# Kernel tuning notes

Measured on AMD Instinct MI355X. Metric: run time of the kernel, lower is better.

The kernel has to match this reference:

```python
import jax, jax.numpy as jnp
import numpy as np

N_EMBD = 1024
N_HEAD = 16
BLOCK_SIZE = 2048
NEG_INF = -1e10


def _rope_cache(head_dim, max_positions):
    # theta_i = 10000^{-2i/dim}, freqs[t, i] = t * theta_i
    theta = 1.0 / (10000.0 ** (jnp.arange(0, head_dim, 2, dtype=jnp.float32) / head_dim))
    freqs = jnp.arange(max_positions, dtype=jnp.float32)[:, None] * theta[None, :]
    return jnp.cos(freqs), jnp.sin(freqs)  # each (max_positions, head_dim//2)


def _apply_rope(x, cos, sin):
    # x: (B, nh, T, hs) interpreted as interleaved complex pairs
    B, nh, T, hs = x.shape
    xr = x.reshape(B, nh, T, hs // 2, 2)
    x0, x1 = xr[..., 0], xr[..., 1]
    c = cos[:T][None, None, :, :]
    s = sin[:T][None, None, :, :]
    o0 = x0 * c - x1 * s
    o1 = x0 * s + x1 * c
    return jnp.stack([o0, o1], axis=-1).reshape(B, nh, T, hs)


def setup_inputs() -> dict:
    key = jax.random.key(0)
    ks = jax.random.split(key, 9)
    B, T, C = 2, 2048, N_EMBD
    sc = 1.0 / np.sqrt(C)
    return {
        "x": jax.random.normal(ks[0], (B, T, C), jnp.float32),
        "Wq": jax.random.normal(ks[1], (C, C), jnp.float32) * sc,
        "bq": jax.random.normal(ks[2], (C,), jnp.float32) * 0.02,
        "Wk": jax.random.normal(ks[3], (C, C), jnp.float32) * sc,
        "bk": jax.random.normal(ks[4], (C,), jnp.float32) * 0.02,
        "Wv": jax.random.normal(ks[5], (C, C), jnp.float32) * sc,
        "bv": jax.random.normal(ks[6], (C,), jnp.float32) * 0.02,
        "Wp": jax.random.normal(ks[7], (C, C), jnp.float32) * sc,
        "bp": jax.random.normal(ks[8], (C,), jnp.float32) * 0.02,
    }


def reference(x, Wq, bq, Wk, bk, Wv, bv, Wp, bp):
    B, T, C = x.shape
    nh, hs = N_HEAD, C // N_HEAD

    def heads(W, b):
        return (x @ W.T + b).reshape(B, T, nh, hs).transpose(0, 2, 1, 3)

    q = heads(Wq, bq)
    k = heads(Wk, bk)
    v = heads(Wv, bv)

    cos, sin = _rope_cache(hs, BLOCK_SIZE)
    q = _apply_rope(q, cos, sin)
    k = _apply_rope(k, cos, sin)

    att = jnp.einsum("bhqd,bhkd->bhqk", q, k) * (1.0 / np.sqrt(hs))
    causal = jnp.tril(jnp.ones((T, T), dtype=bool))
    att = jnp.where(causal[None, None], att, NEG_INF)
    att = jax.nn.softmax(att, axis=-1)
    y = jnp.einsum("bhqk,bhkd->bhqd", att, v)
    y = y.transpose(0, 2, 1, 3).reshape(B, T, C)
    return y @ Wp.T + bp
```

## Files before the change

kernel.cpp:

```cpp
#include <hip/hip_runtime.h>

typedef __bf16 bf16;
typedef short  s16;
typedef s16   s16x8 __attribute__((ext_vector_type(8)));
typedef bf16  bf16x4 __attribute__((ext_vector_type(4)));
typedef float f32x4 __attribute__((ext_vector_type(4)));

#define B_SZ 2
#define T_SEQ 2048
#define C_DIM 1024
#define NH 16
#define HS 64
#define M_TOT (B_SZ * T_SEQ)

#define NEG_BIG (-30000.0f)
#define LOG2_10000 13.287712379549449f
#define Q_PRESCALE 0.18033688011112042f


__device__ __forceinline__ float san(float x) {
    unsigned u = __float_as_uint(x);
    return ((u & 0x7F800000u) == 0x7F800000u) ? 0.f : x;
}

__device__ __forceinline__ void load16_lds(const bf16* g, void* lds_base) {
    __builtin_amdgcn_global_load_lds(
        (const __attribute__((address_space(1))) void*)g,
        (__attribute__((address_space(3))) void*)lds_base, 16, 0, 0);
}

#define CVT_GRID 8448

__global__ __launch_bounds__(256) void cvt_bf16_kernel(
    const float* __restrict__ x,  const float* __restrict__ wq,
    const float* __restrict__ wk, const float* __restrict__ wv,
    const float* __restrict__ wp,
    bf16* __restrict__ xb, bf16* __restrict__ wqb, bf16* __restrict__ wkb,
    bf16* __restrict__ wvb, bf16* __restrict__ wpb,
    float* __restrict__ cs, float* __restrict__ sn)
{
    const int b = blockIdx.x;
    if (b >= 8192) {
        const int idx = (b - 8192) * 256 + threadIdx.x;
        const int t = idx >> 5, i = idx & 31;
        const float theta = __builtin_exp2f(-(float)(2 * i) * (LOG2_10000 / 64.f));
        const float a = (float)t * theta;
        cs[idx] = san(cosf(a));
        sn[idx] = san(sinf(a));
        return;
    }
    int z, base;
    if (b < 4096) { z = 0; base = b; }
    else          { z = 1 + ((b - 4096) >> 10); base = (b - 4096) & 1023; }

    const float* src = (z == 0) ? x : (z == 1) ? wq : (z == 2) ? wk : (z == 3) ? wv : wp;
    bf16* dst = (z == 0) ? xb : (z == 1) ? wqb : (z == 2) ? wkb : (z == 3) ? wvb : wpb;

    const int i = (base * 256 + threadIdx.x) * 4;
    const float4 v = *(const float4*)(src + i);
    bf16x4 o;
    o[0] = (bf16)v.x; o[1] = (bf16)v.y; o[2] = (bf16)v.z; o[3] = (bf16)v.w;
    *(bf16x4*)(dst + i) = o;
}

#define QSTAGE(bufi, kk)                                                       \
    load16_lds(gA + (kk),               (char*)(sA[bufi]) + w * 1024);         \
    load16_lds(gA + 128 * C_DIM + (kk), (char*)(sA[bufi]) + 8192 + w * 1024);  \
    load16_lds(gB + (kk),               (char*)(sB[bufi]) + w * 1024);         \
    load16_lds(gB + 128 * C_DIM + (kk), (char*)(sB[bufi]) + 8192 + w * 1024);

__global__ __launch_bounds__(512, 2) void qkv_gemm(
    const bf16* __restrict__ X, const bf16* __restrict__ W_all,
    const float* __restrict__ bq, const float* __restrict__ bk,
    const float* __restrict__ bv,
    const float* __restrict__ cs_tab, const float* __restrict__ sn_tab,
    bf16* __restrict__ q_ws, bf16* __restrict__ k_ws, bf16* __restrict__ vt_ws)
{
    __shared__ __attribute__((aligned(16))) bf16 sA[3][256 * 32];
    __shared__ __attribute__((aligned(16))) bf16 sB[3][256 * 32];

    const int m0 = blockIdx.x * 256;
    const int n0 = blockIdx.y * 256;
    const int mode = blockIdx.y >> 2;

    const int t = threadIdx.x;
    const int w = t >> 6;
    const int lane = t & 63;
    const int qd = lane >> 4;
    const int r  = lane & 15;
    const int qs = qd ^ ((r >> 1) & 3);
    const int wm = w >> 2, wn = w & 3;
    const int srow = t >> 2;
    const int scol = ((t & 3) ^ ((t >> 3) & 3)) * 8;
    const bf16* gA = X + (size_t)(m0 + srow) * C_DIM + scol;
    const bf16* gB = W_all + (size_t)(n0 + srow) * C_DIM + scol;

    f32x4 acc[8][4] = {};

    QSTAGE(0, 0)
    QSTAGE(1, 32)
    #pragma unroll
    for (int kt_ = 0; kt_ < 32; kt_++) {
        __builtin_amdgcn_sched_barrier(0);
        if (kt_ < 30) asm volatile("s_waitcnt vmcnt(4) lgkmcnt(0)" ::: "memory");
        else          asm volatile("s_waitcnt vmcnt(0) lgkmcnt(0)" ::: "memory");
        __builtin_amdgcn_sched_barrier(0);
        __builtin_amdgcn_s_barrier();
        __builtin_amdgcn_sched_barrier(0);
        if (kt_ + 2 < 32) { QSTAGE((kt_ + 2) % 3, (kt_ + 2) * 32) }
        {
            const bf16* pA = sA[kt_ % 3];
            const bf16* pB = sB[kt_ % 3];
            s16x8 af[8], bfr[4];
            #pragma unroll
            for (int mt = 0; mt < 8; mt++)
                af[mt] = *(const s16x8*)(pA + (wm * 128 + mt * 16 + r) * 32 + qs * 8);
            #pragma unroll
            for (int nt = 0; nt < 4; nt++)
                bfr[nt] = *(const s16x8*)(pB + (wn * 64 + nt * 16 + r) * 32 + qs * 8);
            #pragma unroll
            for (int mt = 0; mt < 8; mt++)
                #pragma unroll
                for (int nt = 0; nt < 4; nt++)
                    acc[mt][nt] = __builtin_amdgcn_mfma_f32_16x16x32_bf16(
                        af[mt], bfr[nt], acc[mt][nt], 0, 0, 0);
        }
    }

    const float* bias = (mode == 0) ? bq : (mode == 1) ? bk : bv;

    if (mode == 2) {
        #pragma unroll
        for (int mt = 0; mt < 8; mt++) {
            const int mrow0 = m0 + wm * 128 + mt * 16 + qd * 4;
            const int bb = mrow0 >> 11;
            const int t0 = mrow0 & 2047;
            #pragma unroll
            for (int nt = 0; nt < 4; nt++) {
                const int cm = (n0 & 1023) + wn * 64 + nt * 16 + r;
                const int h = cm >> 6, d = cm & 63;
                const float bv_ = bias[cm];
                bf16x4 pk;
                #pragma unroll
                for (int reg = 0; reg < 4; reg++)
                    pk[reg] = (bf16)san(acc[mt][nt][reg] + bv_);
                *(bf16x4*)(vt_ws + ((size_t)(bb * NH + h) * HS + d) * T_SEQ + t0) = pk;
            }
        }
    } else {
        bf16* out = (mode == 0) ? q_ws : k_ws;
        const float post = (mode == 0) ? Q_PRESCALE : 1.0f;
        #pragma unroll
        for (int mt = 0; mt < 8; mt++) {
            const int mrow0 = m0 + wm * 128 + mt * 16 + qd * 4;
            const int bb = mrow0 >> 11;
            const int t0 = mrow0 & 2047;
            #pragma unroll
            for (int nt = 0; nt < 4; nt++) {
                const int cm = (n0 & 1023) + wn * 64 + nt * 16 + r;
                const int h = cm >> 6, d = cm & 63;
                const int pi = d >> 1;
                const float bv_ = bias[cm];
                #pragma unroll
                for (int reg = 0; reg < 4; reg++) {
                    const int tt = t0 + reg;
                    float v = san(acc[mt][nt][reg] + bv_);
                    float partner = __shfl_xor(v, 1);
                    float c = cs_tab[tt * 32 + pi];
                    float s = sn_tab[tt * 32 + pi];
                    float rot = (d & 1) ? (v * c + partner * s)
                                        : (v * c - partner * s);
                    out[((size_t)(bb * NH + h) * T_SEQ + tt) * HS + d] =
                        (bf16)san(rot * post);
                }
            }
        }
    }
}

#define STAGE3(bufi, kk)                                                       \
    load16_lds(gA0 + (kk), (char*)(sA + (bufi) * 2048) + w * 1024);            \
    load16_lds(gB0 + (kk), (char*)(sB + (bufi) * 4096) + w * 1024);            \
    load16_lds(gB1 + (kk), (char*)(sB + (bufi) * 4096) + 4096 + w * 1024);

#define K_STEP3(bufi)                                                          \
    {                                                                          \
        const bf16* pA = sA + (bufi) * 2048;                                   \
        const bf16* pB = sB + (bufi) * 4096;                                   \
        s16x8 af[2], bfr[4];                                                   \
        _Pragma("unroll")                                                      \
        for (int mt = 0; mt < 2; mt++)                                         \
            af[mt] = *(const s16x8*)(pA + (wm * 32 + mt * 16 + r) * 32 + qs * 8); \
        _Pragma("unroll")                                                      \
        for (int nt = 0; nt < 4; nt++)                                         \
            bfr[nt] = *(const s16x8*)(pB + (wn * 64 + nt * 16 + r) * 32 + qs * 8); \
        _Pragma("unroll")                                                      \
        for (int mt = 0; mt < 2; mt++)                                         \
            _Pragma("unroll")                                                  \
            for (int nt = 0; nt < 4; nt++)                                     \
                acc[mt][nt] = __builtin_amdgcn_mfma_f32_16x16x32_bf16(         \
                    af[mt], bfr[nt], acc[mt][nt], 0, 0, 0);                    \
    }

#define GEMM_CORE(Xp, Wp_)                                                     \
    const int t = threadIdx.x;                                                 \
    const int w = t >> 6;                                                      \
    const int lane = t & 63;                                                   \
    const int qd = lane >> 4;                                                  \
    const int r  = lane & 15;                                                  \
    const int qs = qd ^ ((r >> 1) & 3);                                        \
    const int wm = w & 1, wn = w >> 1;                                         \
    const int srow = t >> 2;                                                   \
    const int scol = ((t & 3) ^ ((t >> 3) & 3)) * 8;                           \
    const bf16* gA0 = (Xp) + (size_t)(m0 + srow) * C_DIM + scol;               \
    const bf16* gB0 = (Wp_) + (size_t)(n0 + srow) * C_DIM + scol;              \
    const bf16* gB1 = (Wp_) + (size_t)(n0 + 64 + srow) * C_DIM + scol;         \
    f32x4 acc[2][4] = {};                                                      \
    STAGE3(0, 0)                                                               \
    STAGE3(1, 32)                                                              \
    _Pragma("unroll")                                                          \
    for (int kt_ = 0; kt_ < 32; kt_++) {                                       \
        __builtin_amdgcn_sched_barrier(0);                                     \
        if (kt_ < 30) asm volatile("s_waitcnt vmcnt(3) lgkmcnt(0)" ::: "memory"); \
        else          asm volatile("s_waitcnt vmcnt(0) lgkmcnt(0)" ::: "memory"); \
        __builtin_amdgcn_sched_barrier(0);                                     \
        __builtin_amdgcn_s_barrier();                                          \
        __builtin_amdgcn_sched_barrier(0);                                     \
        if (kt_ + 2 < 32) { STAGE3((kt_ + 2) % 3, (kt_ + 2) * 32) }            \
        K_STEP3(kt_ % 3)                                                       \
    }

__global__ __launch_bounds__(256) void proj_gemm(
    const bf16* __restrict__ Y, const bf16* __restrict__ Wp,
    const float* __restrict__ bp, float* __restrict__ out)
{
    __shared__ __attribute__((aligned(16))) bf16 sA[3 * 64 * 32];
    __shared__ __attribute__((aligned(16))) bf16 sB[3 * 128 * 32];

    const int m0 = blockIdx.x * 64;
    const int n0 = blockIdx.y * 128;

    GEMM_CORE(Y, Wp)

    #pragma unroll
    for (int mt = 0; mt < 2; mt++) {
        const int mrow0 = m0 + wm * 32 + mt * 16 + qd * 4;
        #pragma unroll
        for (int nt = 0; nt < 4; nt++) {
            const int col = n0 + wn * 64 + nt * 16 + r;
            const float bv_ = bp[col];
            #pragma unroll
            for (int reg = 0; reg < 4; reg++)
                out[(size_t)(mrow0 + reg) * C_DIM + col] = san(acc[mt][nt][reg] + bv_);
        }
    }
}

__global__ __launch_bounds__(256) void attn_kernel(
    const bf16* __restrict__ q_ws, const bf16* __restrict__ k_ws,
    const bf16* __restrict__ vt_ws, bf16* __restrict__ y_ws)
{
    __shared__ __attribute__((aligned(16))) bf16 sK[2][2][64][32];
    __shared__ __attribute__((aligned(16))) bf16 sV[2][64][32];
    __shared__ __attribute__((aligned(16))) bf16 sP[4][16][72];

    const int id = (int)blockIdx.x;
    const int qt = 31 - (id >> 5);
    const int j  = id & 31;
    const int bh = (j & 7) + 8 * (j >> 3);

    const int w    = threadIdx.x >> 6;
    const int lane = threadIdx.x & 63;
    const int qd = lane >> 4;
    const int r  = lane & 15;
    const int qs = qd ^ ((r >> 1) & 3);
    const int ps = 4 * (r & 3);

    const bf16* Qb = q_ws + (size_t)bh * T_SEQ * HS;
    const bf16* Kb = k_ws + (size_t)bh * T_SEQ * HS;
    const bf16* Vb = vt_ws + (size_t)bh * HS * T_SEQ;

    const int srow = lane >> 2;
    const int scol = ((lane & 3) ^ ((lane >> 3) & 3)) * 8;
    const bf16* Kb_w = Kb + (size_t)(w * 16 + srow) * HS + scol;
    const bf16* Vb_w = Vb + (size_t)(w * 16 + srow) * T_SEQ + scol;

    bf16 (*pw)[72] = sP[w];
    const int bb = bh >> 4, h = bh & 15;

    const int q0 = qt * 64 + w * 16;

    s16x8 aq0 = *(const s16x8*)(Qb + (size_t)(q0 + r) * HS + qd * 8);
    s16x8 aq1 = *(const s16x8*)(Qb + (size_t)(q0 + r) * HS + 32 + qd * 8);

    const s16x8 ones = {(s16)0x3F80, (s16)0x3F80, (s16)0x3F80, (s16)0x3F80,
                        (s16)0x3F80, (s16)0x3F80, (s16)0x3F80, (s16)0x3F80};

    f32x4 o[4] = {};
    f32x4 o_l  = {};

    load16_lds(Kb_w,      &sK[0][0][w * 16][0]);
    load16_lds(Kb_w + 32, &sK[0][1][w * 16][0]);

    for (int kt = 0; kt <= qt; kt++) {
        const int cur = kt & 1;

        __builtin_amdgcn_sched_barrier(0);
        asm volatile("s_waitcnt vmcnt(0) lgkmcnt(0)" ::: "memory");
        __builtin_amdgcn_sched_barrier(0);
        __builtin_amdgcn_s_barrier();
        __builtin_amdgcn_sched_barrier(0);

        {
            const bf16* vp = Vb_w + kt * 64;
            load16_lds(vp,      &sV[0][w * 16][0]);
            load16_lds(vp + 32, &sV[1][w * 16][0]);
        }
        if (kt < qt) {
            const bf16* kp = Kb_w + (size_t)(kt + 1) * 64 * HS;
            load16_lds(kp,      &sK[cur ^ 1][0][w * 16][0]);
            load16_lds(kp + 32, &sK[cur ^ 1][1][w * 16][0]);
        }

        f32x4 s[4];
        __builtin_amdgcn_s_setprio(1);
        #pragma unroll
        for (int c = 0; c < 4; c++) {
            s16x8 k0 = *(const s16x8*)&sK[cur][0][c * 16 + r][qs * 8];
            s16x8 k1 = *(const s16x8*)&sK[cur][1][c * 16 + r][qs * 8];
            f32x4 z = {};
            z = __builtin_amdgcn_mfma_f32_16x16x32_bf16(k0, aq0, z, 0, 0, 0);
            z = __builtin_amdgcn_mfma_f32_16x16x32_bf16(k1, aq1, z, 0, 0, 0);
            s[c] = z;
        }
        __builtin_amdgcn_s_setprio(0);

        if (kt == qt) {
            const int qg = q0 + r;
            #pragma unroll
            for (int c = 0; c < 4; c++)
                #pragma unroll
                for (int reg = 0; reg < 4; reg++) {
                    const int kg = kt * 64 + c * 16 + qd * 4 + reg;
                    s[c][reg] = (kg <= qg) ? s[c][reg] : NEG_BIG;
                }
        }

        #pragma unroll
        for (int c = 0; c < 4; c++) {
            bf16x4 pk;
            #pragma unroll
            for (int reg = 0; reg < 4; reg++)
                pk[reg] = (bf16)__builtin_exp2f(s[c][reg]);
            *(bf16x4*)&pw[r][((4 * c + qd) ^ ps) * 4] = pk;
        }

        __builtin_amdgcn_sched_barrier(0);
        if (kt < qt) asm volatile("s_waitcnt vmcnt(2)" ::: "memory");
        else         asm volatile("s_waitcnt vmcnt(0)" ::: "memory");
        __builtin_amdgcn_sched_barrier(0);
        __builtin_amdgcn_s_barrier();
        __builtin_amdgcn_sched_barrier(0);

        s16x8 ap0 = *(const s16x8*)&pw[r][((2 * qd) ^ ps) * 4];
        s16x8 ap1 = *(const s16x8*)&pw[r][((8 + 2 * qd) ^ ps) * 4];
        __builtin_amdgcn_s_setprio(1);
        o_l = __builtin_amdgcn_mfma_f32_16x16x32_bf16(ones, ap0, o_l, 0, 0, 0);
        o_l = __builtin_amdgcn_mfma_f32_16x16x32_bf16(ones, ap1, o_l, 0, 0, 0);
        #pragma unroll
        for (int nt = 0; nt < 4; nt++) {
            s16x8 av0 = *(const s16x8*)&sV[0][nt * 16 + r][qs * 8];
            s16x8 av1 = *(const s16x8*)&sV[1][nt * 16 + r][qs * 8];
            o[nt] = __builtin_amdgcn_mfma_f32_16x16x32_bf16(av0, ap0, o[nt], 0, 0, 0);
            o[nt] = __builtin_amdgcn_mfma_f32_16x16x32_bf16(av1, ap1, o[nt], 0, 0, 0);
        }
        __builtin_amdgcn_s_setprio(0);
    }

    const float inv = 1.f / fmaxf(o_l[0], 1e-20f);

    const int q = q0 + r;
    bf16* dst = y_ws + ((size_t)(bb * T_SEQ + q) * NH + h) * HS;
    #pragma unroll
    for (int nt = 0; nt < 4; nt++) {
        bf16x4 pk;
        #pragma unroll
        for (int reg = 0; reg < 4; reg++)
            pk[reg] = (bf16)san(o[nt][reg] * inv);
        *(bf16x4*)(dst + nt * 16 + qd * 4) = pk;
    }
}

extern "C" void kernel_launch(void* const* d_in, const int* in_sizes, int n_in,
                              void* d_out, int out_size, void* d_ws, size_t ws_size,
                              hipStream_t stream)
{
    const size_t MB = 1024 * 1024;
    const size_t NEED = 40 * MB + 2 * 65536 * sizeof(float);
    if (ws_size < NEED || n_in < 9) return;

    const float* x  = (const float*)d_in[0];
    const float* Wq = (const float*)d_in[1];
    const float* bq = (const float*)d_in[2];
    const float* Wk = (const float*)d_in[3];
    const float* bk = (const float*)d_in[4];
    const float* Wv = (const float*)d_in[5];
    const float* bv = (const float*)d_in[6];
    const float* Wp = (const float*)d_in[7];
    const float* bp = (const float*)d_in[8];
    float* out = (float*)d_out;

    char* ws = (char*)d_ws;
    bf16*  q_ws   = (bf16*)(ws + 0 * MB);
    bf16*  k_ws   = (bf16*)(ws + 8 * MB);
    bf16*  vt_ws  = (bf16*)(ws + 16 * MB);
    bf16*  x_b    = (bf16*)(ws + 24 * MB);
    bf16*  y_ws   = (bf16*)(ws + 24 * MB);
    bf16*  Wq_b   = (bf16*)(ws + 32 * MB);
    bf16*  Wk_b   = (bf16*)(ws + 34 * MB);
    bf16*  Wv_b   = (bf16*)(ws + 36 * MB);
    bf16*  Wp_b   = (bf16*)(ws + 38 * MB);
    float* cs_tab = (float*)(ws + 40 * MB);
    float* sn_tab = cs_tab + 65536;
    const bf16* W_all = Wq_b;

    cvt_bf16_kernel<<<dim3(CVT_GRID), 256, 0, stream>>>(
        x, Wq, Wk, Wv, Wp, x_b, Wq_b, Wk_b, Wv_b, Wp_b, cs_tab, sn_tab);
    qkv_gemm<<<dim3(M_TOT / 256, 3 * C_DIM / 256), 512, 0, stream>>>(
        x_b, W_all, bq, bk, bv, cs_tab, sn_tab, q_ws, k_ws, vt_ws);
    attn_kernel<<<dim3(32 * 32), 256, 0, stream>>>(
        q_ws, k_ws, vt_ws, y_ws);
    proj_gemm<<<dim3(M_TOT / 64, C_DIM / 128), 256, 0, stream>>>(
        y_ws, Wp_b, bp, out);
}
```

Measured before the change: 182.6 us.

## Software-pipeline attention loop: overlap QK softmax of tile kt with PV of tile kt-1

Restructures the attention loop into a skewed pipeline. Each iteration computes QK^T and exp for the current key tile, then runs the PV MFMAs for the previous tile. V and P buffers are double-buffered, which removes the second barrier inside the loop. The goal is to overlap exp/VALU work with MFMA work and cut one synchronisation per iteration, at the cost of more LDS and a prologue/epilogue.

```diff
diff --git a/kernel.cpp b/kernel.cpp
--- a/kernel.cpp
+++ b/kernel.cpp
@@ -256,13 +256,70 @@
     }
 }
 
+
+#define ATT_QKSM(ktv, kb, pb)                                                  \
+    {                                                                          \
+        f32x4 s_[4];                                                           \
+        __builtin_amdgcn_s_setprio(1);                                         \
+        _Pragma("unroll")                                                      \
+        for (int c = 0; c < 4; c++) {                                          \
+            s16x8 k0 = *(const s16x8*)&sK[kb][0][c * 16 + r][qs * 8];          \
+            s16x8 k1 = *(const s16x8*)&sK[kb][1][c * 16 + r][qs * 8];          \
+            f32x4 z = {};                                                      \
+            z = __builtin_amdgcn_mfma_f32_16x16x32_bf16(k0, aq0, z, 0, 0, 0);  \
+            z = __builtin_amdgcn_mfma_f32_16x16x32_bf16(k1, aq1, z, 0, 0, 0);  \
+            s_[c] = z;                                                         \
+        }                                                                      \
+        __builtin_amdgcn_s_setprio(0);                                         \
+        if ((ktv) == qt) {                                                     \
+            const int qg = q0 + r;                                             \
+            _Pragma("unroll")                                                  \
+            for (int c = 0; c < 4; c++)                                        \
+                _Pragma("unroll")                                              \
+                for (int reg = 0; reg < 4; reg++) {                            \
+                    const int kg = (ktv) * 64 + c * 16 + qd * 4 + reg;         \
+                    s_[c][reg] = (kg <= qg) ? s_[c][reg] : NEG_BIG;            \
+                }                                                              \
+        }                                                                      \
+        _Pragma("unroll")                                                      \
+        for (int c = 0; c < 4; c++) {                                          \
+            bf16x4 pk;                                                         \
+            _Pragma("unroll")                                                  \
+            for (int reg = 0; reg < 4; reg++)                                  \
+                pk[reg] = (bf16)__builtin_exp2f(s_[c][reg]);                   \
+            *(bf16x4*)&sP[pb][w][r][((4 * c + qd) ^ ps) * 4] = pk;             \
+        }                                                                      \
+    }
+
+#define ATT_PV(ap0_, ap1_, vb)                                                 \
+    {                                                                          \
+        __builtin_amdgcn_s_setprio(1);                                         \
+        o_l = __builtin_amdgcn_mfma_f32_16x16x32_bf16(ones, ap0_, o_l, 0, 0, 0); \
+        o_l = __builtin_amdgcn_mfma_f32_16x16x32_bf16(ones, ap1_, o_l, 0, 0, 0); \
+        _Pragma("unroll")                                                      \
+        for (int nt = 0; nt < 4; nt++) {                                       \
+            s16x8 av0 = *(const s16x8*)&sV[vb][0][nt * 16 + r][qs * 8];        \
+            s16x8 av1 = *(const s16x8*)&sV[vb][1][nt * 16 + r][qs * 8];        \
+            o[nt] = __builtin_amdgcn_mfma_f32_16x16x32_bf16(av0, ap0_, o[nt], 0, 0, 0); \
+            o[nt] = __builtin_amdgcn_mfma_f32_16x16x32_bf16(av1, ap1_, o[nt], 0, 0, 0); \
+        }                                                                      \
+        __builtin_amdgcn_s_setprio(0);                                         \
+    }
+
+#define ATT_DRAIN_BARRIER()                                                    \
+    __builtin_amdgcn_sched_barrier(0);                                         \
+    asm volatile("s_waitcnt vmcnt(0) lgkmcnt(0)" ::: "memory");                \
+    __builtin_amdgcn_sched_barrier(0);                                         \
+    __builtin_amdgcn_s_barrier();                                              \
+    __builtin_amdgcn_sched_barrier(0);
+
 __global__ __launch_bounds__(256) void attn_kernel(
     const bf16* __restrict__ q_ws, const bf16* __restrict__ k_ws,
     const bf16* __restrict__ vt_ws, bf16* __restrict__ y_ws)
 {
     __shared__ __attribute__((aligned(16))) bf16 sK[2][2][64][32];
-    __shared__ __attribute__((aligned(16))) bf16 sV[2][64][32];
-    __shared__ __attribute__((aligned(16))) bf16 sP[4][16][72];
+    __shared__ __attribute__((aligned(16))) bf16 sV[2][2][64][32];
+    __shared__ __attribute__((aligned(16))) bf16 sP[2][4][16][72];
 
     const int id = (int)blockIdx.x;
     const int qt = 31 - (id >> 5);
@@ -285,9 +342,7 @@
     const bf16* Kb_w = Kb + (size_t)(w * 16 + srow) * HS + scol;
     const bf16* Vb_w = Vb + (size_t)(w * 16 + srow) * T_SEQ + scol;
 
-    bf16 (*pw)[72] = sP[w];
     const int bb = bh >> 4, h = bh & 15;
-
     const int q0 = qt * 64 + w * 16;
 
     s16x8 aq0 = *(const s16x8*)(Qb + (size_t)(q0 + r) * HS + qd * 8);
@@ -301,20 +356,24 @@
 
     load16_lds(Kb_w,      &sK[0][0][w * 16][0]);
     load16_lds(Kb_w + 32, &sK[0][1][w * 16][0]);
-
-    for (int kt = 0; kt <= qt; kt++) {
+    ATT_DRAIN_BARRIER()
+    load16_lds(Vb_w,      &sV[0][0][w * 16][0]);
+    load16_lds(Vb_w + 32, &sV[0][1][w * 16][0]);
+    if (qt > 0) {
+        const bf16* kp = Kb_w + (size_t)64 * HS;
+        load16_lds(kp,      &sK[1][0][w * 16][0]);
+        load16_lds(kp + 32, &sK[1][1][w * 16][0]);
+    }
+    ATT_QKSM(0, 0, 0)
+
+    for (int kt = 1; kt <= qt; kt++) {
         const int cur = kt & 1;
-
-        __builtin_amdgcn_sched_barrier(0);
-        asm volatile("s_waitcnt vmcnt(0) lgkmcnt(0)" ::: "memory");
-        __builtin_amdgcn_sched_barrier(0);
-        __builtin_amdgcn_s_barrier();
-        __builtin_amdgcn_sched_barrier(0);
+        ATT_DRAIN_BARRIER()
 
         {
             const bf16* vp = Vb_w + kt * 64;
-            load16_lds(vp,      &sV[0][w * 16][0]);
-            load16_lds(vp + 32, &sV[1][w * 16][0]);
+            load16_lds(vp,      &sV[cur][0][w * 16][0]);
+            load16_lds(vp + 32, &sV[cur][1][w * 16][0]);
         }
         if (kt < qt) {
             const bf16* kp = Kb_w + (size_t)(kt + 1) * 64 * HS;
@@ -322,59 +381,19 @@
             load16_lds(kp + 32, &sK[cur ^ 1][1][w * 16][0]);
         }
 
-        f32x4 s[4];
-        __builtin_amdgcn_s_setprio(1);
-        #pragma unroll
-        for (int c = 0; c < 4; c++) {
-            s16x8 k0 = *(const s16x8*)&sK[cur][0][c * 16 + r][qs * 8];
-            s16x8 k1 = *(const s16x8*)&sK[cur][1][c * 16 + r][qs * 8];
-            f32x4 z = {};
-            z = __builtin_amdgcn_mfma_f32_16x16x32_bf16(k0, aq0, z, 0, 0, 0);
-            z = __builtin_amdgcn_mfma_f32_16x16x32_bf16(k1, aq1, z, 0, 0, 0);
-            s[c] = z;
-        }
-        __builtin_amdgcn_s_setprio(0);
-
-        if (kt == qt) {
-            const int qg = q0 + r;
-            #pragma unroll
-            for (int c = 0; c < 4; c++)
-                #pragma unroll
-                for (int reg = 0; reg < 4; reg++) {
-                    const int kg = kt * 64 + c * 16 + qd * 4 + reg;
-                    s[c][reg] = (kg <= qg) ? s[c][reg] : NEG_BIG;
-                }
-        }
-
-        #pragma unroll
-        for (int c = 0; c < 4; c++) {
-            bf16x4 pk;
-            #pragma unroll
-            for (int reg = 0; reg < 4; reg++)
-                pk[reg] = (bf16)__builtin_exp2f(s[c][reg]);
-            *(bf16x4*)&pw[r][((4 * c + qd) ^ ps) * 4] = pk;
-        }
-
-        __builtin_amdgcn_sched_barrier(0);
-        if (kt < qt) asm volatile("s_waitcnt vmcnt(2)" ::: "memory");
-        else         asm volatile("s_waitcnt vmcnt(0)" ::: "memory");
-        __builtin_amdgcn_sched_barrier(0);
-        __builtin_amdgcn_s_barrier();
-        __builtin_amdgcn_sched_barrier(0);
-
-        s16x8 ap0 = *(const s16x8*)&pw[r][((2 * qd) ^ ps) * 4];
-        s16x8 ap1 = *(const s16x8*)&pw[r][((8 + 2 * qd) ^ ps) * 4];
-        __builtin_amdgcn_s_setprio(1);
-        o_l = __builtin_amdgcn_mfma_f32_16x16x32_bf16(ones, ap0, o_l, 0, 0, 0);
-        o_l = __builtin_amdgcn_mfma_f32_16x16x32_bf16(ones, ap1, o_l, 0, 0, 0);
-        #pragma unroll
-        for (int nt = 0; nt < 4; nt++) {
-            s16x8 av0 = *(const s16x8*)&sV[0][nt * 16 + r][qs * 8];
-            s16x8 av1 = *(const s16x8*)&sV[1][nt * 16 + r][qs * 8];
-            o[nt] = __builtin_amdgcn_mfma_f32_16x16x32_bf16(av0, ap0, o[nt], 0, 0, 0);
-            o[nt] = __builtin_amdgcn_mfma_f32_16x16x32_bf16(av1, ap1, o[nt], 0, 0, 0);
-        }
-        __builtin_amdgcn_s_setprio(0);
+        s16x8 ap0 = *(const s16x8*)&sP[cur ^ 1][w][r][((2 * qd) ^ ps) * 4];
+        s16x8 ap1 = *(const s16x8*)&sP[cur ^ 1][w][r][((8 + 2 * qd) ^ ps) * 4];
+
+        ATT_QKSM(kt, cur, cur)
+        ATT_PV(ap0, ap1, cur ^ 1)
+    }
+
+    ATT_DRAIN_BARRIER()
+    {
+        const int pb = qt & 1;
+        s16x8 ap0 = *(const s16x8*)&sP[pb][w][r][((2 * qd) ^ ps) * 4];
+        s16x8 ap1 = *(const s16x8*)&sP[pb][w][r][((8 + 2 * qd) ^ ps) * 4];
+        ATT_PV(ap0, ap1, pb)
     }
 
     const float inv = 1.f / fmaxf(o_l[0], 1e-20f);
```

Result: no change. 180.5 us (-1.1%).
